# Optimization experiments

Hardware: AMD Instinct MI355X
Metric: run time of the kernel (lower is better)

The kernel has to match this reference:

```python
import jax, jax.numpy as jnp
import numpy as np

NTOKEN = 100000
NINP = 64
N_EDGES = 600000
BATCH = 64
MAX_LEN = 200


def gcn_conv(x, W, b, edge_index, num_nodes):
    # PyG GCNConv: add self-loops, symmetric normalization, x @ W then propagate.
    src, dst = edge_index[0], edge_index[1]
    loop = jnp.arange(num_nodes, dtype=src.dtype)
    src = jnp.concatenate([src, loop])
    dst = jnp.concatenate([dst, loop])
    deg = jax.ops.segment_sum(jnp.ones_like(dst, dtype=x.dtype), dst,
                              num_segments=num_nodes)
    dinv = jnp.where(deg > 0, deg ** -0.5, 0.0)
    norm = dinv[src] * dinv[dst]                      # [E+N]
    h = x @ W                                         # [N, out]
    out = jax.ops.segment_sum(h[src] * norm[:, None], dst,
                              num_segments=num_nodes)  # [N, out]
    return out + b


def setup_inputs() -> dict:
    key = jax.random.key(0)
    k_emb, k_w1, k_w2, k_e, k_in = jax.random.split(key, 5)
    # Xavier-normal scaled params
    emb = jax.random.normal(k_emb, (NTOKEN, NINP), jnp.float32) * (2.0 / (NTOKEN + NINP)) ** 0.5
    emb = emb.at[0].set(0.0)  # padding_idx=0
    W1 = jax.random.normal(k_w1, (NINP, 2 * NINP), jnp.float32) * (2.0 / (3 * NINP)) ** 0.5
    b1 = jnp.zeros((2 * NINP,), jnp.float32)
    W2 = jax.random.normal(k_w2, (2 * NINP, NINP), jnp.float32) * (2.0 / (3 * NINP)) ** 0.5
    b2 = jnp.zeros((NINP,), jnp.float32)
    edge_index = jax.random.randint(k_e, (2, N_EDGES), 0, NTOKEN, dtype=jnp.int32)
    inp = jax.random.randint(k_in, (BATCH, MAX_LEN), 0, NTOKEN, dtype=jnp.int32)
    return {"input": inp, "emb": emb, "W1": W1, "b1": b1,
            "W2": W2, "b2": b2, "edge_index": edge_index}


def reference(input, emb, W1, b1, W2, b2, edge_index):
    # GraphNN forward (eval mode: dropout = identity, no activation between convs)
    h = gcn_conv(emb, W1, b1, edge_index, NTOKEN)          # [N, 2*ninp]
    lookup = gcn_conv(h, W2, b2, edge_index, NTOKEN)       # [N, ninp]
    # one-hot scatter + einsum('bt,td->bd') is exactly a row gather:
    out = lookup[input]                                    # [B, L, ninp]
    return out
```

## Files before the change

### kernel.cpp

```cpp
#include <hip/hip_runtime.h>
#include <hip/hip_fp16.h>
#include <math.h>

static constexpr int NTOK = 100000;
static constexpr int NE   = 600000;
static constexpr int NPOS = 64 * 200;
static constexpr int NBKT = 196;
static constexpr int BCAP = 5120;
static constexpr int EPB  = 2344;
static constexpr int EPT  = 10;
static constexpr int NCVT = (NTOK * 8 + 255) / 256;

typedef unsigned long long ull;

__device__ __forceinline__ float2 h2f(unsigned int u) {
    __half2 h = *reinterpret_cast<__half2*>(&u);
    return __half22float2(h);
}
__device__ __forceinline__ unsigned int f2h(float a, float b) {
    __half2 h = __floats2half2_rn(a, b);
    return *reinterpret_cast<unsigned int*>(&h);
}
__device__ __forceinline__ float u16f(unsigned short x) {
    __half h = *reinterpret_cast<__half*>(&x);
    return __half2float(h);
}

__global__ void k_setup(int* __restrict__ bucketCnt) {
    bucketCnt[threadIdx.x] = 0;
}

__global__ __launch_bounds__(256) void
k_bucket(const int* __restrict__ ei, int* __restrict__ bucketCnt,
         ull* __restrict__ buckets,
         const float4* __restrict__ W14, const float* __restrict__ b1,
         const float4* __restrict__ W24, float4* __restrict__ W124,
         float4* __restrict__ bw4,
         const float4* __restrict__ emb4, uint4* __restrict__ embh4) {
    __shared__ int cnt[256];
    __shared__ int pref[256];
    __shared__ int eoff[256];
    __shared__ int base[256];
    __shared__ ull stg[EPB];
    int t = threadIdx.x;

    if (blockIdx.x >= 260) {
        int i = (blockIdx.x - 260) * 256 + t;
        if (i < NTOK * 8) {
            float4 a = emb4[2 * i];
            float4 b = emb4[2 * i + 1];
            uint4 o;
            o.x = f2h(a.x, a.y); o.y = f2h(a.z, a.w);
            o.z = f2h(b.x, b.y); o.w = f2h(b.z, b.w);
            embh4[i] = o;
        }
        return;
    }
    if (blockIdx.x >= 256) {
        int blk = blockIdx.x - 256;
        int j4 = t & 15;
        int k = blk * 16 + (t >> 4);
        float4 acc = {0.f, 0.f, 0.f, 0.f};
        for (int mq = 0; mq < 32; ++mq) {
            float4 a = W14[k * 32 + mq];
            float4 w0 = W24[(4 * mq + 0) * 16 + j4];
            float4 w1 = W24[(4 * mq + 1) * 16 + j4];
            float4 w2 = W24[(4 * mq + 2) * 16 + j4];
            float4 w3 = W24[(4 * mq + 3) * 16 + j4];
            acc.x += a.x * w0.x + a.y * w1.x + a.z * w2.x + a.w * w3.x;
            acc.y += a.x * w0.y + a.y * w1.y + a.z * w2.y + a.w * w3.y;
            acc.z += a.x * w0.z + a.y * w1.z + a.z * w2.z + a.w * w3.z;
            acc.w += a.x * w0.w + a.y * w1.w + a.z * w2.w + a.w * w3.w;
        }
        W124[k * 16 + j4] = acc;
        if (blk == 0 && t < 16) {
            float4 b = {0.f, 0.f, 0.f, 0.f};
            for (int m = 0; m < 128; ++m) {
                float a = b1[m];
                float4 w = W24[m * 16 + t];
                b.x += a * w.x; b.y += a * w.y; b.z += a * w.z; b.w += a * w.w;
            }
            bw4[t] = b;
        }
        return;
    }

    cnt[t] = 0;
    __syncthreads();

    int e0 = blockIdx.x * EPB;
    int eEnd = e0 + EPB; if (eEnd > NE) eEnd = NE;
    int tot = eEnd - e0;

    int s_[EPT], d_[EPT], r_[EPT];
#pragma unroll
    for (int k = 0; k < EPT; ++k) {
        int i = e0 + t + k * 256;
        s_[k] = -1;
        if (i < eEnd) {
            s_[k] = ei[i];
            d_[k] = ei[NE + i];
            r_[k] = atomicAdd(&cnt[d_[k] >> 9], 1);
        }
    }
    __syncthreads();

    int v = cnt[t];
    pref[t] = v;
    __syncthreads();
    for (int o = 1; o < 256; o <<= 1) {
        int x = pref[t];
        if (t >= o) x += pref[t - o];
        __syncthreads();
        pref[t] = x;
        __syncthreads();
    }
    eoff[t] = pref[t] - v;
    base[t] = (v > 0) ? atomicAdd(&bucketCnt[t], v) : 0;
    __syncthreads();

#pragma unroll
    for (int k = 0; k < EPT; ++k) {
        if (s_[k] >= 0) {
            int b = d_[k] >> 9;
            stg[eoff[b] + r_[k]] =
                ((ull)(unsigned)s_[k] << 32) | (unsigned)d_[k];
        }
    }
    __syncthreads();

    for (int i = t; i < tot; i += 256) {
        ull e = stg[i];
        int b = ((int)(unsigned)e) >> 9;
        int off = base[b] + (i - eoff[b]);
        if (off < BCAP) buckets[(long)b * BCAP + off] = e;
    }
}

__global__ __launch_bounds__(256) void
k_csrbuild(const ull* __restrict__ buckets, const int* __restrict__ bucketCnt,
           int* __restrict__ csr, int* __restrict__ roff, int* __restrict__ degs,
           float* __restrict__ dinv, float* __restrict__ dinv2) {
    __shared__ int cnt[512];
    __shared__ int pref[512];
    __shared__ int cur[512];
    __shared__ int bsum[256];
    __shared__ int stg[BCAP];
    int t = threadIdx.x;
    cnt[t] = 0; cnt[t + 256] = 0;
    __syncthreads();

    int b = blockIdx.x;
    int n0 = b << 9;
    int m = bucketCnt[b]; if (m > BCAP) m = BCAP;
    const ull* bb = buckets + (long)b * BCAP;

    for (int i = t; i < m; i += 256) {
        int dd = (int)(unsigned)bb[i];
        atomicAdd(&cnt[dd - n0], 1);
    }
    __syncthreads();

    int a0 = cnt[2 * t], a1 = cnt[2 * t + 1];
    bsum[t] = a0 + a1;
    __syncthreads();
    for (int o = 1; o < 256; o <<= 1) {
        int x = bsum[t];
        if (t >= o) x += bsum[t - o];
        __syncthreads();
        bsum[t] = x;
        __syncthreads();
    }
    int eb = bsum[t] - (a0 + a1);
    pref[2 * t] = eb;          cur[2 * t] = eb;
    pref[2 * t + 1] = eb + a0; cur[2 * t + 1] = eb + a0;
    __syncthreads();

    for (int i = t; i < m; i += 256) {
        ull v = bb[i];
        int dd = (int)(unsigned)v;
        int ss = (int)(v >> 32);
        int pos = atomicAdd(&cur[dd - n0], 1);
        stg[pos] = ss;
    }
    __syncthreads();

    for (int i = t; i < m; i += 256) csr[(long)b * BCAP + i] = stg[i];

#pragma unroll
    for (int k = 0; k < 2; ++k) {
        int l = t + k * 256;
        int n = n0 + l;
        if (n < NTOK) {
            int dg = cnt[l];
            degs[n] = dg;
            roff[n] = b * BCAP + pref[l];
            float dd = rsqrtf((float)dg + 1.0f);
            dinv[n] = dd;
            dinv2[n] = dd * dd;
        }
    }
}

__global__ void k_gatherA(const int* __restrict__ csr, const int* __restrict__ roff,
                          const int* __restrict__ degs,
                          const float* __restrict__ dinv, const uint4* __restrict__ eh4,
                          uint4* __restrict__ u4, float* __restrict__ s_raw) {
    int idx = blockIdx.x * 256 + threadIdx.x;
    int n = idx >> 3;
    if (n >= NTOK) return;
    int jq = idx & 7;
    int d = degs[n];
    const int* row = csr + roff[n];

    float a[8];
    float cn = dinv[n];
    {
        uint4 v = eh4[((long)n << 3) + jq];
        float2 f0 = h2f(v.x), f1 = h2f(v.y), f2 = h2f(v.z), f3 = h2f(v.w);
        a[0] = cn * f0.x; a[1] = cn * f0.y; a[2] = cn * f1.x; a[3] = cn * f1.y;
        a[4] = cn * f2.x; a[5] = cn * f2.y; a[6] = cn * f3.x; a[7] = cn * f3.y;
    }
    float sdv = cn;
    int e = 0;
    for (; e + 4 <= d; e += 4) {
        int s0 = row[e], s1 = row[e + 1], s2 = row[e + 2], s3 = row[e + 3];
        float c0 = dinv[s0], c1 = dinv[s1], c2 = dinv[s2], c3 = dinv[s3];
        uint4 v0 = eh4[((long)s0 << 3) + jq];
        uint4 v1 = eh4[((long)s1 << 3) + jq];
        uint4 v2 = eh4[((long)s2 << 3) + jq];
        uint4 v3 = eh4[((long)s3 << 3) + jq];
        {
            float2 f0 = h2f(v0.x), f1 = h2f(v0.y), f2 = h2f(v0.z), f3 = h2f(v0.w);
            a[0] += c0 * f0.x; a[1] += c0 * f0.y; a[2] += c0 * f1.x; a[3] += c0 * f1.y;
            a[4] += c0 * f2.x; a[5] += c0 * f2.y; a[6] += c0 * f3.x; a[7] += c0 * f3.y;
        }
        {
            float2 f0 = h2f(v1.x), f1 = h2f(v1.y), f2 = h2f(v1.z), f3 = h2f(v1.w);
            a[0] += c1 * f0.x; a[1] += c1 * f0.y; a[2] += c1 * f1.x; a[3] += c1 * f1.y;
            a[4] += c1 * f2.x; a[5] += c1 * f2.y; a[6] += c1 * f3.x; a[7] += c1 * f3.y;
        }
        {
            float2 f0 = h2f(v2.x), f1 = h2f(v2.y), f2 = h2f(v2.z), f3 = h2f(v2.w);
            a[0] += c2 * f0.x; a[1] += c2 * f0.y; a[2] += c2 * f1.x; a[3] += c2 * f1.y;
            a[4] += c2 * f2.x; a[5] += c2 * f2.y; a[6] += c2 * f3.x; a[7] += c2 * f3.y;
        }
        {
            float2 f0 = h2f(v3.x), f1 = h2f(v3.y), f2 = h2f(v3.z), f3 = h2f(v3.w);
            a[0] += c3 * f0.x; a[1] += c3 * f0.y; a[2] += c3 * f1.x; a[3] += c3 * f1.y;
            a[4] += c3 * f2.x; a[5] += c3 * f2.y; a[6] += c3 * f3.x; a[7] += c3 * f3.y;
        }
        sdv += (c0 + c1) + (c2 + c3);
    }
    for (; e < d; ++e) {
        int sx = row[e];
        float c = dinv[sx];
        uint4 v = eh4[((long)sx << 3) + jq];
        float2 f0 = h2f(v.x), f1 = h2f(v.y), f2 = h2f(v.z), f3 = h2f(v.w);
        a[0] += c * f0.x; a[1] += c * f0.y; a[2] += c * f1.x; a[3] += c * f1.y;
        a[4] += c * f2.x; a[5] += c * f2.y; a[6] += c * f3.x; a[7] += c * f3.y;
        sdv += c;
    }
    uint4 o;
    o.x = f2h(a[0], a[1]); o.y = f2h(a[2], a[3]);
    o.z = f2h(a[4], a[5]); o.w = f2h(a[6], a[7]);
    u4[((long)n << 3) + jq] = o;
    if (jq == 0) s_raw[n] = sdv;
}

__global__ __launch_bounds__(256) void
k_fused(const int* __restrict__ inp, const int* __restrict__ csr,
        const int* __restrict__ roff, const int* __restrict__ degs,
        const float* __restrict__ dinv, const float* __restrict__ dinv2,
        const float* __restrict__ s_raw, const unsigned short* __restrict__ uh,
        const float* __restrict__ W12, const float* __restrict__ bw,
        const float* __restrict__ b2, float* __restrict__ out) {
    __shared__ float w[64 * 64];
    int tid = threadIdx.x;
    {
        const float4* W4 = (const float4*)W12;
        float4* w4 = (float4*)w;
        for (int i = tid; i < 1024; i += 256) w4[i] = W4[i];
    }
    __syncthreads();

    int lane = tid & 63;
    int wid  = tid >> 6;
    int p = blockIdx.x * 4 + wid;
    int t = inp[p];
    int d = degs[t];
    const int* row = csr + roff[t];

    float z = dinv2[t] * u16f(uh[((long)t << 6) + lane]);
    int e = 0;
    for (; e + 4 <= d; e += 4) {
        int s0 = row[e], s1 = row[e + 1], s2 = row[e + 2], s3 = row[e + 3];
        float c0 = dinv2[s0], c1 = dinv2[s1], c2 = dinv2[s2], c3 = dinv2[s3];
        float u0 = u16f(uh[((long)s0 << 6) + lane]);
        float u1 = u16f(uh[((long)s1 << 6) + lane]);
        float u2 = u16f(uh[((long)s2 << 6) + lane]);
        float u3 = u16f(uh[((long)s3 << 6) + lane]);
        z += (c0 * u0 + c1 * u1) + (c2 * u2 + c3 * u3);
    }
    for (; e < d; ++e) {
        int sx = row[e];
        z += dinv2[sx] * u16f(uh[((long)sx << 6) + lane]);
    }
    z *= dinv[t];

    float o0 = 0.f, o1 = 0.f, o2 = 0.f, o3 = 0.f;
#pragma unroll
    for (int k = 0; k < 64; k += 4) {
        float z0 = __uint_as_float(__builtin_amdgcn_readlane(__float_as_uint(z), k));
        float z1 = __uint_as_float(__builtin_amdgcn_readlane(__float_as_uint(z), k + 1));
        float z2 = __uint_as_float(__builtin_amdgcn_readlane(__float_as_uint(z), k + 2));
        float z3 = __uint_as_float(__builtin_amdgcn_readlane(__float_as_uint(z), k + 3));
        o0 += z0 * w[(k + 0) * 64 + lane];
        o1 += z1 * w[(k + 1) * 64 + lane];
        o2 += z2 * w[(k + 2) * 64 + lane];
        o3 += z3 * w[(k + 3) * 64 + lane];
    }
    float o = (o0 + o1) + (o2 + o3) + dinv[t] * s_raw[t] * bw[lane] + b2[lane];
    out[((long)p << 6) + lane] = o;
}

extern "C" void kernel_launch(void* const* d_in, const int* in_sizes, int n_in,
                              void* d_out, int out_size, void* d_ws, size_t ws_size,
                              hipStream_t stream) {
    const int*   inp = (const int*)d_in[0];
    const float* emb = (const float*)d_in[1];
    const float* W1  = (const float*)d_in[2];
    const float* b1  = (const float*)d_in[3];
    const float* W2  = (const float*)d_in[4];
    const float* b2  = (const float*)d_in[5];
    const int*   ei  = (const int*)d_in[6];
    float* out = (float*)d_out;

    char* ws = (char*)d_ws;
    int*   bucketCnt = (int*)(ws + 0);
    float* W12   = (float*)(ws + 4096);
    float* bw    = (float*)(ws + 20480);
    int*   degs  = (int*)(ws + 24576);
    float* dinv  = (float*)(ws + 424576);
    float* dinv2 = (float*)(ws + 824576);
    float* s_raw = (float*)(ws + 1224576);
    int*   roff  = (int*)(ws + 1624576);
    ull*   buckets = (ull*)(ws + 2024576);
    int*   csr   = (int*)(ws + 10052736);
    unsigned short* embh = (unsigned short*)(ws + 14066816);
    unsigned short* u    = (unsigned short*)(ws + 26866816);

    k_setup<<<1, 256, 0, stream>>>(bucketCnt);

    k_bucket<<<260 + NCVT, 256, 0, stream>>>(
        ei, bucketCnt, buckets,
        (const float4*)W1, b1, (const float4*)W2, (float4*)W12, (float4*)bw,
        (const float4*)emb, (uint4*)embh);

    k_csrbuild<<<NBKT, 256, 0, stream>>>(buckets, bucketCnt, csr, roff,
                                         degs, dinv, dinv2);

    int gblk = (NTOK * 8 + 255) / 256;
    k_gatherA<<<gblk, 256, 0, stream>>>(csr, roff, degs, dinv, (const uint4*)embh,
                                        (uint4*)u, s_raw);

    k_fused<<<NPOS / 4, 256, 0, stream>>>(inp, csr, roff, degs, dinv, dinv2,
                                          s_raw, u, W12, bw, b2, out);
}
```

Measured before the change: 67.20 us.

## Restrict first-layer gather to nodes reachable from queried tokens

Marks the tokens referenced by the input, then marks every source neighbor of those tokens while building the CSR, and compacts the flags into a worklist. The first-layer aggregation kernel then processes only worklist nodes instead of all 100k nodes. This is exact because the output only needs the 2-hop neighbourhood of the queried tokens. It adds a zeroing pass over the flag arrays, an extra compaction launch, and scattered flag writes in the CSR build, and the first-layer output is left stale for nodes not on the worklist.

```diff
diff --git a/kernel.cpp b/kernel.cpp
--- a/kernel.cpp
+++ b/kernel.cpp
@@ -9,7 +9,9 @@
 static constexpr int BCAP = 5120;
 static constexpr int EPB  = 2344;
 static constexpr int EPT  = 10;
+static constexpr int NFLG = (NPOS + 255) / 256;
 static constexpr int NCVT = (NTOK * 8 + 255) / 256;
+static constexpr int ZERO4 = 804864 / 16;
 
 typedef unsigned long long ull;
 
@@ -26,8 +28,9 @@
     return __half2float(h);
 }
 
-__global__ void k_setup(int* __restrict__ bucketCnt) {
-    bucketCnt[threadIdx.x] = 0;
+__global__ void k_setup(int4* __restrict__ p) {
+    int i = blockIdx.x * 256 + threadIdx.x;
+    if (i < ZERO4) p[i] = {0, 0, 0, 0};
 }
 
 __global__ __launch_bounds__(256) void
@@ -36,6 +39,8 @@
          const float4* __restrict__ W14, const float* __restrict__ b1,
          const float4* __restrict__ W24, float4* __restrict__ W124,
          float4* __restrict__ bw4,
+         const int* __restrict__ inp, int* __restrict__ flagT,
+         int* __restrict__ flagU,
          const float4* __restrict__ emb4, uint4* __restrict__ embh4) {
     __shared__ int cnt[256];
     __shared__ int pref[256];
@@ -44,8 +49,8 @@
     __shared__ ull stg[EPB];
     int t = threadIdx.x;
 
-    if (blockIdx.x >= 260) {
-        int i = (blockIdx.x - 260) * 256 + t;
+    if (blockIdx.x >= 260 + NFLG) {
+        int i = (blockIdx.x - 260 - NFLG) * 256 + t;
         if (i < NTOK * 8) {
             float4 a = emb4[2 * i];
             float4 b = emb4[2 * i + 1];
@@ -53,6 +58,15 @@
             o.x = f2h(a.x, a.y); o.y = f2h(a.z, a.w);
             o.z = f2h(b.x, b.y); o.w = f2h(b.z, b.w);
             embh4[i] = o;
+        }
+        return;
+    }
+    if (blockIdx.x >= 260) {
+        int p = (blockIdx.x - 260) * 256 + t;
+        if (p < NPOS) {
+            int tok = inp[p];
+            flagT[tok] = 1;
+            flagU[tok] = 1;
         }
         return;
     }
@@ -140,24 +154,35 @@
 __global__ __launch_bounds__(256) void
 k_csrbuild(const ull* __restrict__ buckets, const int* __restrict__ bucketCnt,
            int* __restrict__ csr, int* __restrict__ roff, int* __restrict__ degs,
-           float* __restrict__ dinv, float* __restrict__ dinv2) {
+           float* __restrict__ dinv, float* __restrict__ dinv2,
+           const int* __restrict__ flagT, int* __restrict__ flagU) {
     __shared__ int cnt[512];
     __shared__ int pref[512];
     __shared__ int cur[512];
     __shared__ int bsum[256];
+    __shared__ int ftl[512];
     __shared__ int stg[BCAP];
     int t = threadIdx.x;
     cnt[t] = 0; cnt[t + 256] = 0;
-    __syncthreads();
 
     int b = blockIdx.x;
     int n0 = b << 9;
+    {
+        int n = n0 + t;
+        ftl[t] = (n < NTOK) ? flagT[n] : 0;
+        n = n0 + t + 256;
+        ftl[t + 256] = (n < NTOK) ? flagT[n] : 0;
+    }
+    __syncthreads();
+
     int m = bucketCnt[b]; if (m > BCAP) m = BCAP;
     const ull* bb = buckets + (long)b * BCAP;
 
     for (int i = t; i < m; i += 256) {
-        int dd = (int)(unsigned)bb[i];
+        ull v = bb[i];
+        int dd = (int)(unsigned)v;
         atomicAdd(&cnt[dd - n0], 1);
+        if (ftl[dd - n0]) flagU[(int)(v >> 32)] = 1;
     }
     __syncthreads();
 
@@ -202,13 +227,31 @@
     }
 }
 
-__global__ void k_gatherA(const int* __restrict__ csr, const int* __restrict__ roff,
+__global__ void k_compact(const int* __restrict__ flagU, int* __restrict__ wl,
+                          int* __restrict__ wl_n) {
+    int n = blockIdx.x * 256 + threadIdx.x;
+    int lane = threadIdx.x & 63;
+    int f = (n < NTOK) ? flagU[n] : 0;
+    unsigned long long m = __ballot(f != 0);
+    int cw = __popcll(m);
+    int base = 0;
+    if (lane == 0 && cw) base = atomicAdd(wl_n, cw);
+    base = __builtin_amdgcn_readfirstlane(base);
+    if (f) {
+        int pos = base + __popcll(m & ((1ULL << lane) - 1));
+        wl[pos] = n;
+    }
+}
+
+__global__ void k_gatherA(const int* __restrict__ wl, const int* __restrict__ wl_n,
+                          const int* __restrict__ csr, const int* __restrict__ roff,
                           const int* __restrict__ degs,
                           const float* __restrict__ dinv, const uint4* __restrict__ eh4,
                           uint4* __restrict__ u4, float* __restrict__ s_raw) {
     int idx = blockIdx.x * 256 + threadIdx.x;
-    int n = idx >> 3;
-    if (n >= NTOK) return;
+    int wi = idx >> 3;
+    if (wi >= wl_n[0]) return;
+    int n = wl[wi];
     int jq = idx & 7;
     int d = degs[n];
     const int* row = csr + roff[n];
@@ -338,31 +381,37 @@
 
     char* ws = (char*)d_ws;
     int*   bucketCnt = (int*)(ws + 0);
-    float* W12   = (float*)(ws + 4096);
-    float* bw    = (float*)(ws + 20480);
-    int*   degs  = (int*)(ws + 24576);
-    float* dinv  = (float*)(ws + 424576);
-    float* dinv2 = (float*)(ws + 824576);
-    float* s_raw = (float*)(ws + 1224576);
-    int*   roff  = (int*)(ws + 1624576);
-    ull*   buckets = (ull*)(ws + 2024576);
-    int*   csr   = (int*)(ws + 10052736);
-    unsigned short* embh = (unsigned short*)(ws + 14066816);
-    unsigned short* u    = (unsigned short*)(ws + 26866816);
-
-    k_setup<<<1, 256, 0, stream>>>(bucketCnt);
-
-    k_bucket<<<260 + NCVT, 256, 0, stream>>>(
+    int*   wl_n  = (int*)(ws + 1024);
+    int*   flagT = (int*)(ws + 4096);
+    int*   flagU = (int*)(ws + 404096);
+    float* W12   = (float*)(ws + 804864);
+    float* bw    = (float*)(ws + 821248);
+    int*   degs  = (int*)(ws + 821504);
+    float* dinv  = (float*)(ws + 1221504);
+    float* dinv2 = (float*)(ws + 1621504);
+    float* s_raw = (float*)(ws + 2021504);
+    int*   roff  = (int*)(ws + 2421504);
+    int*   wl    = (int*)(ws + 2821504);
+    ull*   buckets = (ull*)(ws + 3221504);
+    int*   csr   = (int*)(ws + 11249664);
+    unsigned short* embh = (unsigned short*)(ws + 15263744);
+    unsigned short* u    = (unsigned short*)(ws + 28063744);
+
+    k_setup<<<(ZERO4 + 255) / 256, 256, 0, stream>>>((int4*)ws);
+
+    k_bucket<<<260 + NFLG + NCVT, 256, 0, stream>>>(
         ei, bucketCnt, buckets,
         (const float4*)W1, b1, (const float4*)W2, (float4*)W12, (float4*)bw,
-        (const float4*)emb, (uint4*)embh);
+        inp, flagT, flagU, (const float4*)emb, (uint4*)embh);
 
     k_csrbuild<<<NBKT, 256, 0, stream>>>(buckets, bucketCnt, csr, roff,
-                                         degs, dinv, dinv2);
+                                         degs, dinv, dinv2, flagT, flagU);
+
+    k_compact<<<(NTOK + 255) / 256, 256, 0, stream>>>(flagU, wl, wl_n);
 
     int gblk = (NTOK * 8 + 255) / 256;
-    k_gatherA<<<gblk, 256, 0, stream>>>(csr, roff, degs, dinv, (const uint4*)embh,
-                                        (uint4*)u, s_raw);
+    k_gatherA<<<gblk, 256, 0, stream>>>(wl, wl_n, csr, roff, degs, dinv,
+                                        (const uint4*)embh, (uint4*)u, s_raw);
 
     k_fused<<<NPOS / 4, 256, 0, stream>>>(inp, csr, roff, degs, dinv, dinv2,
                                           s_raw, u, W12, bw, b2, out);
```

Measured after the change: 83.49 us. 1.24x slower.
